# Kernel optimization log

Hardware: AMD Instinct MI355X
Metric: run time of the kernel (lower is better)

Reference implementation:

```python
import jax, jax.numpy as jnp
import numpy as np

N_NODES = 50000
D = 128
L = 3  # layers
R = 4  # relations
E = 200000  # edges per relation
LN_EPS = 1e-5
NEG_SLOPE = 0.2


def setup_inputs() -> dict:
    key = jax.random.key(0)
    ks = jax.random.split(key, 12)
    s = 1.0 / np.sqrt(D)  # xavier-ish scale
    return {
        "h": jax.random.normal(ks[0], (N_NODES, D), jnp.float32),
        "edge_src": jax.random.randint(ks[1], (R, E), 0, N_NODES, jnp.int32),
        "edge_dst": jax.random.randint(ks[2], (R, E), 0, N_NODES, jnp.int32),
        "W_src": jax.random.normal(ks[3], (L, R, D, D), jnp.float32) * s,
        "W_dst": jax.random.normal(ks[4], (L, R, D, D), jnp.float32) * s,
        "attn_l": jax.random.normal(ks[5], (L, R, D), jnp.float32) * s,
        "attn_r": jax.random.normal(ks[6], (L, R, D), jnp.float32) * s,
        "gat_bias": jax.random.normal(ks[7], (L, R, D), jnp.float32) * 0.02,
        "ntype_bias": jax.random.normal(ks[8], (L, D), jnp.float32) * 0.02,
        "ln_gamma": jnp.ones((L, D), jnp.float32),
        "ln_beta": jnp.zeros((L, D), jnp.float32),
    }


def _gat_rel(x, Wsrc, Wdst, al, ar, b, src, dst):
    # single-head DGL GATConv with bipartite (src, dst) feats (same node set here)
    n = x.shape[0]
    hs = x @ Wsrc  # [N, D] projected source feats
    hd = x @ Wdst  # [N, D] projected dest feats
    el = (hs * al).sum(-1)  # [N]
    er = (hd * ar).sum(-1)  # [N]
    e = jax.nn.leaky_relu(el[src] + er[dst], NEG_SLOPE)  # [E]
    # edge softmax over incoming edges of each dst node
    m = jax.lax.stop_gradient(jax.ops.segment_max(e, dst, num_segments=n))
    a = jnp.exp(e - m[dst])
    denom = jax.ops.segment_sum(a, dst, num_segments=n)
    w = a / denom[dst]  # [E] attention weights
    out = jax.ops.segment_sum(hs[src] * w[:, None], dst, num_segments=n)  # [N, D]
    return out + b


def _layer_norm(x, g, b):
    mu = x.mean(-1, keepdims=True)
    var = ((x - mu) ** 2).mean(-1, keepdims=True)
    return (x - mu) * jax.lax.rsqrt(var + LN_EPS) * g + b


def reference(h, edge_src, edge_dst, W_src, W_dst, attn_l, attn_r,
              gat_bias, ntype_bias, ln_gamma, ln_beta):
    x = h
    n_layers = W_src.shape[0]
    gat_vmapped = jax.vmap(_gat_rel, in_axes=(None, 0, 0, 0, 0, 0, 0, 0))
    for l in range(n_layers):
        rel_out = gat_vmapped(x, W_src[l], W_dst[l], attn_l[l], attn_r[l],
                              gat_bias[l], edge_src, edge_dst)  # [R, N, D]
        hsum = rel_out.sum(0) + ntype_bias[l]  # HeteroGraphConv 'sum' + ntype bias
        if l < n_layers - 1:
            hsum = jax.nn.relu(hsum)  # activation on all but final layer
        # mean over heads (num_heads=1) is identity; then per-layer LayerNorm
        x = _layer_norm(hsum, ln_gamma[l], ln_beta[l])
    return x
```

## Files before the change

kernel.cpp:

```cpp
#include <hip/hip_runtime.h>

#define NN 50000
#define DIM 128
#define NREL 4
#define NEDGE 200000
#define NLAYER 3
#define SNB 196

typedef short s16x8 __attribute__((ext_vector_type(8)));
typedef float f32x4 __attribute__((ext_vector_type(4)));

__device__ __forceinline__ unsigned short f2bf(float f) {
    union { float f; unsigned u; } c; c.f = f;
    unsigned u = c.u + 0x7fffu + ((c.u >> 16) & 1u);
    return (unsigned short)(u >> 16);
}
__device__ __forceinline__ float lo_bf(unsigned u) {
    union { float f; unsigned u; } c; c.u = u << 16; return c.f;
}
__device__ __forceinline__ float hi_bf(unsigned u) {
    union { float f; unsigned u; } c; c.u = u & 0xffff0000u; return c.f;
}

__global__ __launch_bounds__(256) void k_constf(float* __restrict__ out, int n, float v) {
    int i = blockIdx.x * 256 + threadIdx.x;
    if (i < n) out[i] = v;
}

__global__ __launch_bounds__(256) void k_count(const int* __restrict__ dst, int* __restrict__ counts) {
    int r = blockIdx.y;
    int i = blockIdx.x * 256 + threadIdx.x;
    if (i < NEDGE) {
        int d = dst[r * NEDGE + i];
        if ((unsigned)d < NN) atomicAdd(&counts[r * NN + d], 1);
    }
}

__global__ __launch_bounds__(256) void k_s1(const int* __restrict__ counts, int* __restrict__ bsum) {
    int r = blockIdx.y, b = blockIdx.x;
    int i = b * 256 + threadIdx.x;
    int v = (i < NN) ? counts[r * NN + i] : 0;
    #pragma unroll
    for (int m = 1; m < 64; m <<= 1) v += __shfl_xor(v, m);
    __shared__ int ws[4];
    int wid = threadIdx.x >> 6, lane = threadIdx.x & 63;
    if (lane == 0) ws[wid] = v;
    __syncthreads();
    if (threadIdx.x == 0) bsum[r * SNB + b] = ws[0] + ws[1] + ws[2] + ws[3];
}

__global__ __launch_bounds__(256) void k_s2(const int* __restrict__ bsum, int* __restrict__ boff) {
    int r = threadIdx.x >> 6;
    int lane = threadIdx.x & 63;
    int carry = 0;
    for (int c0 = 0; c0 < SNB; c0 += 64) {
        int b = c0 + lane;
        int v = (b < SNB) ? bsum[r * SNB + b] : 0;
        int inc = v;
        #pragma unroll
        for (int d = 1; d < 64; d <<= 1) {
            int t = __shfl_up(inc, d);
            if (lane >= d) inc += t;
        }
        if (b < SNB) boff[r * SNB + b] = carry + inc - v;
        carry += __shfl(inc, 63);
    }
}

__global__ __launch_bounds__(256) void k_s3(const int* __restrict__ counts, const int* __restrict__ boff,
                                            int* __restrict__ row_ptr) {
    int r = blockIdx.y, b = blockIdx.x;
    int i = b * 256 + threadIdx.x;
    int v = (i < NN) ? counts[r * NN + i] : 0;
    int lane = threadIdx.x & 63, wid = threadIdx.x >> 6;
    int inc = v;
    #pragma unroll
    for (int d = 1; d < 64; d <<= 1) {
        int t = __shfl_up(inc, d);
        if (lane >= d) inc += t;
    }
    __shared__ int ws[4];
    if (lane == 63) ws[wid] = inc;
    __syncthreads();
    int woff = 0;
    #pragma unroll
    for (int w = 0; w < 4; ++w) woff += (w < wid) ? ws[w] : 0;
    if (i < NN) row_ptr[r * (NN + 1) + i] = boff[r * SNB + b] + woff + inc - v;
    if (b == 0 && threadIdx.x == 0) row_ptr[r * (NN + 1) + NN] = NEDGE;
}

__global__ __launch_bounds__(256) void k_copynext(const int* __restrict__ row_ptr, int* __restrict__ nxt) {
    int r = blockIdx.y;
    int i = blockIdx.x * 256 + threadIdx.x;
    if (i < NN) nxt[r * NN + i] = row_ptr[r * (NN + 1) + i];
}

__global__ __launch_bounds__(256) void k_fill(const int* __restrict__ src, const int* __restrict__ dst,
                                              int* __restrict__ nxt, int* __restrict__ csr) {
    int r = blockIdx.y;
    int i = blockIdx.x * 256 + threadIdx.x;
    if (i < NEDGE) {
        int d = dst[r * NEDGE + i];
        if ((unsigned)d >= NN) return;
        int pos = atomicAdd(&nxt[r * NN + d], 1);
        if ((unsigned)pos < NEDGE) csr[r * NEDGE + pos] = src[r * NEDGE + i];
    }
}

__global__ __launch_bounds__(256) void k_prep(const float* __restrict__ Wsrc,
                                              const float* __restrict__ Wdst,
                                              const float* __restrict__ al,
                                              const float* __restrict__ ar,
                                              const float* __restrict__ ntb,
                                              const float* __restrict__ gb,
                                              const float* __restrict__ x,
                                              unsigned short* __restrict__ wf,
                                              float* __restrict__ wl,
                                              float* __restrict__ wr,
                                              float* __restrict__ biasc,
                                              unsigned short* __restrict__ xb) {
    int b = blockIdx.x;
    const int PL = NLAYER * 512;
    if (b < PL) {
        int l = b / 512;
        int t = b % 512;
        if (t < 256) {
            int idx = t * 256 + threadIdx.x;
            int jj = idx & 7, lane = (idx >> 3) & 63, s = (idx >> 9) & 3, tt = (idx >> 11) & 7, r = idx >> 14;
            int k = s * 32 + ((lane >> 4) << 3) + jj;
            int n = tt * 16 + (lane & 15);
            wf[l * 65536 + idx] = f2bf(Wsrc[((size_t)(l * NREL + r) * DIM + k) * DIM + n]);
        } else if (t < 384) {
            int gw = (t - 256) * 4 + (threadIdx.x >> 6);
            int lane = threadIdx.x & 63;
            int r = gw >> 7, k = gw & 127;
            const float* wrow = Wsrc + (((size_t)(l * NREL + r) * DIM + k) * DIM);
            const float* arow = al + (l * NREL + r) * DIM;
            float s = wrow[lane * 2] * arow[lane * 2] + wrow[lane * 2 + 1] * arow[lane * 2 + 1];
            #pragma unroll
            for (int m = 1; m < 64; m <<= 1) s += __shfl_xor(s, m);
            if (lane == 0) wl[l * 512 + gw] = s;
        } else {
            int gw = (t - 384) * 4 + (threadIdx.x >> 6);
            int lane = threadIdx.x & 63;
            int r = gw >> 7, k = gw & 127;
            const float* wrow = Wdst + (((size_t)(l * NREL + r) * DIM + k) * DIM);
            const float* arow = ar + (l * NREL + r) * DIM;
            float s = wrow[lane * 2] * arow[lane * 2] + wrow[lane * 2 + 1] * arow[lane * 2 + 1];
            #pragma unroll
            for (int m = 1; m < 64; m <<= 1) s += __shfl_xor(s, m);
            if (lane == 0) wr[l * 512 + gw] = s;
        }
    } else if (b < PL + 2) {
        int t = (b - PL) * 256 + threadIdx.x;
        if (t < NLAYER * DIM) {
            int l = t >> 7, k = t & 127;
            float s = ntb[t];
            #pragma unroll
            for (int r = 0; r < NREL; ++r) s += gb[(l * NREL + r) * DIM + k];
            biasc[t] = s;
        }
    } else {
        int i = ((b - PL - 2) * 256 + threadIdx.x) * 4;
        f32x4 v = *(const f32x4*)(x + i);
        unsigned short o[4];
        #pragma unroll
        for (int j = 0; j < 4; ++j) o[j] = f2bf(v[j]);
        *(ushort2*)(xb + i) = make_ushort2(o[0], o[1]);
        *(ushort2*)(xb + i + 2) = make_ushort2(o[2], o[3]);
    }
}

__global__ __launch_bounds__(256) void k_er0(const float* __restrict__ x,
                                             const float* __restrict__ wl,
                                             const float* __restrict__ wr,
                                             float* __restrict__ el,
                                             float* __restrict__ er) {
    int oct = threadIdx.x >> 3, ol = threadIdx.x & 7;
    int n = blockIdx.x * 32 + oct;
    if (n >= NN) return;
    int f0 = ol * 16;
    const float* xp = x + (size_t)n * DIM + f0;
    f32x4 xv[4];
    #pragma unroll
    for (int k = 0; k < 4; ++k) xv[k] = *(const f32x4*)(xp + 4 * k);
    #pragma unroll
    for (int r = 0; r < NREL; ++r) {
        float sl = 0.f, sr = 0.f;
        #pragma unroll
        for (int k = 0; k < 4; ++k) {
            f32x4 lv = *(const f32x4*)(wl + r * DIM + f0 + 4 * k);
            f32x4 rv = *(const f32x4*)(wr + r * DIM + f0 + 4 * k);
            sl += xv[k][0] * lv[0] + xv[k][1] * lv[1] + xv[k][2] * lv[2] + xv[k][3] * lv[3];
            sr += xv[k][0] * rv[0] + xv[k][1] * rv[1] + xv[k][2] * rv[2] + xv[k][3] * rv[3];
        }
        sl += __shfl_xor(sl, 1); sl += __shfl_xor(sl, 2); sl += __shfl_xor(sl, 4);
        sr += __shfl_xor(sr, 1); sr += __shfl_xor(sr, 2); sr += __shfl_xor(sr, 4);
        if (ol == 0) { el[r * NN + n] = sl; er[r * NN + n] = sr; }
    }
}

__global__ __launch_bounds__(256) void k_fused(const unsigned short* __restrict__ xb,
                                               const float* __restrict__ el,
                                               const float* __restrict__ er,
                                               const int* __restrict__ row_ptr,
                                               const int* __restrict__ csr,
                                               const unsigned short* __restrict__ wf,
                                               const float* __restrict__ biasc,
                                               const float* __restrict__ lng,
                                               const float* __restrict__ lnb,
                                               const float* __restrict__ wl,
                                               const float* __restrict__ wr,
                                               float* __restrict__ dout,
                                               unsigned short* __restrict__ xb2,
                                               float* __restrict__ el2,
                                               float* __restrict__ er2,
                                               int l, int last) {
    __shared__ s16x8 lds_a[16 * 64];
    int tid = threadIdx.x;

    {
        int pair = tid >> 2;
        int ol   = tid & 3;
        int nd   = pair >> 2;
        int r    = pair & 3;
        int n    = blockIdx.x * 16 + nd;
        int f0   = ol * 32;

        int start = row_ptr[r * (NN + 1) + n];
        int end   = row_ptr[r * (NN + 1) + n + 1];
        if (start < 0) start = 0;
        if (end > NEDGE) end = NEDGE;
        int deg = end - start;

        float ern = er[r * NN + n];
        const int* cp = csr + r * NEDGE;
        const float* elp = el + r * NN;

        f32x4 av[8] = {{0,0,0,0},{0,0,0,0},{0,0,0,0},{0,0,0,0},
                       {0,0,0,0},{0,0,0,0},{0,0,0,0},{0,0,0,0}};
        float denom = 0.f;
        if (deg > 0) {
            int s0 = cp[start]; if ((unsigned)s0 >= NN) s0 = 0;
            float e0 = elp[s0];
            const uint4* hp = (const uint4*)(xb + (size_t)s0 * DIM + f0);
            uint4 xa = hp[0], xbv = hp[1], xc = hp[2], xd = hp[3];
            for (int e = 0; e < deg; ++e) {
                int i1 = start + e + 1; i1 = (i1 < end) ? i1 : start;
                int s1 = cp[i1]; if ((unsigned)s1 >= NN) s1 = 0;
                float e1 = elp[s1];
                const uint4* hp1 = (const uint4*)(xb + (size_t)s1 * DIM + f0);
                uint4 ya = hp1[0], yb = hp1[1], yc = hp1[2], yd = hp1[3];

                float ev = e0 + ern;
                ev = ev >= 0.f ? ev : 0.2f * ev;
                ev = fminf(fmaxf(ev, -60.f), 60.f);
                float p = __expf(ev);
                denom += p;
                av[0][0] += p * lo_bf(xa.x); av[0][1] += p * hi_bf(xa.x);
                av[0][2] += p * lo_bf(xa.y); av[0][3] += p * hi_bf(xa.y);
                av[1][0] += p * lo_bf(xa.z); av[1][1] += p * hi_bf(xa.z);
                av[1][2] += p * lo_bf(xa.w); av[1][3] += p * hi_bf(xa.w);
                av[2][0] += p * lo_bf(xbv.x); av[2][1] += p * hi_bf(xbv.x);
                av[2][2] += p * lo_bf(xbv.y); av[2][3] += p * hi_bf(xbv.y);
                av[3][0] += p * lo_bf(xbv.z); av[3][1] += p * hi_bf(xbv.z);
                av[3][2] += p * lo_bf(xbv.w); av[3][3] += p * hi_bf(xbv.w);
                av[4][0] += p * lo_bf(xc.x); av[4][1] += p * hi_bf(xc.x);
                av[4][2] += p * lo_bf(xc.y); av[4][3] += p * hi_bf(xc.y);
                av[5][0] += p * lo_bf(xc.z); av[5][1] += p * hi_bf(xc.z);
                av[5][2] += p * lo_bf(xc.w); av[5][3] += p * hi_bf(xc.w);
                av[6][0] += p * lo_bf(xd.x); av[6][1] += p * hi_bf(xd.x);
                av[6][2] += p * lo_bf(xd.y); av[6][3] += p * hi_bf(xd.y);
                av[7][0] += p * lo_bf(xd.z); av[7][1] += p * hi_bf(xd.z);
                av[7][2] += p * lo_bf(xd.w); av[7][3] += p * hi_bf(xd.w);
                e0 = e1; xa = ya; xbv = yb; xc = yc; xd = yd;
            }
        }
        float inv = (deg > 0) ? (1.0f / denom) : 0.f;
        #pragma unroll
        for (int q = 0; q < 4; ++q) {
            s16x8 o;
            #pragma unroll
            for (int j = 0; j < 4; ++j) {
                o[j]     = (short)f2bf(av[2 * q][j] * inv);
                o[j + 4] = (short)f2bf(av[2 * q + 1][j] * inv);
            }
            lds_a[(r * 4 + ol) * 64 + q * 16 + nd] = o;
        }
    }
    __syncthreads();

    int wv = tid >> 6, lane = tid & 63;
    int quad = lane >> 4, n16 = lane & 15;
    f32x4 acc0 = {0.f, 0.f, 0.f, 0.f}, acc1 = {0.f, 0.f, 0.f, 0.f};
    {
        const s16x8* wfp = (const s16x8*)wf + (size_t)l * NREL * 2048;
        int t0c = wv * 2, t1c = wv * 2 + 1;
        #pragma unroll
        for (int sp = 0; sp < 16; ++sp) {
            s16x8 a = lds_a[sp * 64 + lane];
            const s16x8* wb = wfp + (size_t)(sp >> 2) * 2048;
            int sl = sp & 3;
            s16x8 b0 = wb[(t0c * 4 + sl) * 64 + lane];
            s16x8 b1 = wb[(t1c * 4 + sl) * 64 + lane];
            acc0 = __builtin_amdgcn_mfma_f32_16x16x32_bf16(a, b0, acc0, 0, 0, 0);
            acc1 = __builtin_amdgcn_mfma_f32_16x16x32_bf16(a, b1, acc1, 0, 0, 0);
        }
    }
    __syncthreads();
    float* Cl = (float*)lds_a;
    {
        int t0c = wv * 2, t1c = wv * 2 + 1;
        #pragma unroll
        for (int reg = 0; reg < 4; ++reg) {
            int row = quad * 4 + reg;
            Cl[row * DIM + t0c * 16 + n16] = acc0[reg];
            Cl[row * DIM + t1c * 16 + n16] = acc1[reg];
        }
    }
    __syncthreads();

    {
        int nd2 = tid >> 4;
        int sub = tid & 15;
        int f   = sub * 8;
        int n2  = blockIdx.x * 16 + nd2;

        float t[8];
        #pragma unroll
        for (int j = 0; j < 8; ++j) t[j] = Cl[nd2 * DIM + f + j] + biasc[l * DIM + f + j];
        if (!last) {
            #pragma unroll
            for (int j = 0; j < 8; ++j) t[j] = fmaxf(t[j], 0.f);
        }
        float s1 = 0.f;
        #pragma unroll
        for (int j = 0; j < 8; ++j) s1 += t[j];
        s1 += __shfl_xor(s1, 1); s1 += __shfl_xor(s1, 2);
        s1 += __shfl_xor(s1, 4); s1 += __shfl_xor(s1, 8);
        float mean = s1 * (1.0f / 128.0f);
        float s2 = 0.f;
        #pragma unroll
        for (int j = 0; j < 8; ++j) { t[j] -= mean; s2 += t[j] * t[j]; }
        s2 += __shfl_xor(s2, 1); s2 += __shfl_xor(s2, 2);
        s2 += __shfl_xor(s2, 4); s2 += __shfl_xor(s2, 8);
        float rs = rsqrtf(s2 * (1.0f / 128.0f) + 1e-5f);

        float y[8];
        #pragma unroll
        for (int j = 0; j < 8; ++j)
            y[j] = t[j] * rs * lng[l * DIM + f + j] + lnb[l * DIM + f + j];

        if (last) {
            float* op = dout + (size_t)n2 * DIM + f;
            f32x4 v0, v1;
            v0[0] = y[0]; v0[1] = y[1]; v0[2] = y[2]; v0[3] = y[3];
            v1[0] = y[4]; v1[1] = y[5]; v1[2] = y[6]; v1[3] = y[7];
            *(f32x4*)op = v0;
            *(f32x4*)(op + 4) = v1;
        } else {
            unsigned pk[4];
            #pragma unroll
            for (int j = 0; j < 4; ++j)
                pk[j] = (unsigned)f2bf(y[2 * j]) | ((unsigned)f2bf(y[2 * j + 1]) << 16);
            uint4 v; v.x = pk[0]; v.y = pk[1]; v.z = pk[2]; v.w = pk[3];
            *(uint4*)(xb2 + (size_t)n2 * DIM + f) = v;

            const float* wlp = wl + (l + 1) * 512;
            const float* wrp = wr + (l + 1) * 512;
            #pragma unroll
            for (int rp = 0; rp < NREL; ++rp) {
                float sl_ = 0.f, sr_ = 0.f;
                #pragma unroll
                for (int j = 0; j < 8; ++j) {
                    sl_ += y[j] * wlp[rp * DIM + f + j];
                    sr_ += y[j] * wrp[rp * DIM + f + j];
                }
                sl_ += __shfl_xor(sl_, 1); sl_ += __shfl_xor(sl_, 2);
                sl_ += __shfl_xor(sl_, 4); sl_ += __shfl_xor(sl_, 8);
                sr_ += __shfl_xor(sr_, 1); sr_ += __shfl_xor(sr_, 2);
                sr_ += __shfl_xor(sr_, 4); sr_ += __shfl_xor(sr_, 8);
                if (sub == 0) {
                    el2[rp * NN + n2] = sl_;
                    er2[rp * NN + n2] = sr_;
                }
            }
        }
    }
}

extern "C" void kernel_launch(void* const* d_in, const int* in_sizes, int n_in,
                              void* d_out, int out_size, void* d_ws, size_t ws_size,
                              hipStream_t stream) {
    const float* h        = (const float*)d_in[0];
    const int*   edge_src = (const int*)d_in[1];
    const int*   edge_dst = (const int*)d_in[2];
    const float* W_src    = (const float*)d_in[3];
    const float* W_dst    = (const float*)d_in[4];
    const float* attn_l   = (const float*)d_in[5];
    const float* attn_r   = (const float*)d_in[6];
    const float* gat_bias = (const float*)d_in[7];
    const float* ntype_b  = (const float*)d_in[8];
    const float* ln_g     = (const float*)d_in[9];
    const float* ln_b     = (const float*)d_in[10];

    if (n_in < 11) return;
    if (in_sizes[0] != NN * DIM) return;
    if (in_sizes[1] != NREL * NEDGE || in_sizes[2] != NREL * NEDGE) return;
    if (in_sizes[3] != NLAYER * NREL * DIM * DIM || in_sizes[4] != NLAYER * NREL * DIM * DIM) return;
    if (in_sizes[5] != NLAYER * NREL * DIM || in_sizes[6] != NLAYER * NREL * DIM) return;
    if (in_sizes[7] != NLAYER * NREL * DIM || in_sizes[8] != NLAYER * DIM) return;
    if (out_size != NN * DIM) return;

    auto align256 = [](size_t x) { return (x + 255) & ~(size_t)255; };
    size_t szElEr = align256((size_t)NREL * NN * 4);
    size_t szXbf  = align256((size_t)NN * DIM * 2);
    size_t szWlr  = align256((size_t)NLAYER * 512 * 4);
    size_t szBc   = align256((size_t)NLAYER * DIM * 4);
    size_t szWf   = align256((size_t)NLAYER * NREL * DIM * DIM * 2);
    size_t szRp   = align256((size_t)NREL * (NN + 1) * 4);
    size_t szNxt  = align256((size_t)NREL * NN * 4);
    size_t szCsr  = align256((size_t)NREL * NEDGE * 4);
    size_t szScn  = align256((size_t)NREL * SNB * 4) * 2;
    size_t need = 4 * szElEr + 2 * szXbf + 2 * szWlr + szBc + szWf + szRp + szNxt + szCsr + szScn;

    if (ws_size < need) {
        k_constf<<<(NN * DIM + 255) / 256, 256, 0, stream>>>((float*)d_out, NN * DIM, 100.0f);
        return;
    }

    char* base = (char*)d_ws;
    size_t off = 0;
    auto alloc = [&](size_t bytes) -> char* { char* p = base + off; off += align256(bytes); return p; };

    float* el   = (float*)alloc((size_t)NREL * NN * 4);
    float* er   = (float*)alloc((size_t)NREL * NN * 4);
    float* el2  = (float*)alloc((size_t)NREL * NN * 4);
    float* er2  = (float*)alloc((size_t)NREL * NN * 4);
    unsigned short* xbf  = (unsigned short*)alloc((size_t)NN * DIM * 2);
    unsigned short* xbf2 = (unsigned short*)alloc((size_t)NN * DIM * 2);
    float* wl    = (float*)alloc((size_t)NLAYER * 512 * 4);
    float* wr    = (float*)alloc((size_t)NLAYER * 512 * 4);
    float* biasc = (float*)alloc((size_t)NLAYER * DIM * 4);
    unsigned short* wfrag = (unsigned short*)alloc((size_t)NLAYER * NREL * DIM * DIM * 2);
    int* rowp = (int*)alloc((size_t)NREL * (NN + 1) * 4);
    int* nxt  = (int*)alloc((size_t)NREL * NN * 4);
    int* csr  = (int*)alloc((size_t)NREL * NEDGE * 4);
    int* bsum = (int*)alloc((size_t)NREL * SNB * 4);
    int* boff = (int*)alloc((size_t)NREL * SNB * 4);

    (void)hipMemsetAsync(nxt, 0, (size_t)NREL * NN * 4, stream);
    k_count<<<dim3((NEDGE + 255) / 256, NREL), 256, 0, stream>>>(edge_dst, nxt);
    k_s1<<<dim3(SNB, NREL), 256, 0, stream>>>(nxt, bsum);
    k_s2<<<1, 256, 0, stream>>>(bsum, boff);
    k_s3<<<dim3(SNB, NREL), 256, 0, stream>>>(nxt, boff, rowp);
    k_copynext<<<dim3((NN + 255) / 256, NREL), 256, 0, stream>>>(rowp, nxt);
    k_fill<<<dim3((NEDGE + 255) / 256, NREL), 256, 0, stream>>>(edge_src, edge_dst, nxt, csr);
    k_prep<<<NLAYER * 512 + 2 + NN * DIM / 1024, 256, 0, stream>>>(
        W_src, W_dst, attn_l, attn_r, ntype_b, gat_bias, h, wfrag, wl, wr, biasc, xbf);
    k_er0<<<(NN + 31) / 32, 256, 0, stream>>>(h, wl, wr, el, er);

    float* dout = (float*)d_out;
    k_fused<<<NN / 16, 256, 0, stream>>>(xbf, el, er, rowp, csr, wfrag, biasc, ln_g, ln_b,
                                         wl, wr, dout, xbf2, el2, er2, 0, 0);
    k_fused<<<NN / 16, 256, 0, stream>>>(xbf2, el2, er2, rowp, csr, wfrag, biasc, ln_g, ln_b,
                                         wl, wr, dout, xbf, el, er, 1, 0);
    k_fused<<<NN / 16, 256, 0, stream>>>(xbf, el, er, rowp, csr, wfrag, biasc, ln_g, ln_b,
                                         wl, wr, dout, xbf2, el2, er2, 2, 1);
}
```

Measured before the change: 348.9 us.

## Split edge gather across two lane groups and widen fused kernel to 512 threads

The fused GAT kernel now runs 512 threads per block. Each (node, relation, feature-slice) gets two lanes that take alternating incoming edges, and their partial sums are combined with a cross-lane shuffle. This roughly halves the serial gather chain per lane, giving more memory-level parallelism in the latency-bound aggregation. The MFMA and LayerNorm stages are redistributed across 8 waves to match. The CSR copy kernel is also folded into the scan kernel, saving a launch, at the cost of higher register pressure and extra shuffle reductions.

```diff
diff --git a/kernel.cpp b/kernel.cpp
--- a/kernel.cpp
+++ b/kernel.cpp
@@ -68,7 +68,7 @@
 }
 
 __global__ __launch_bounds__(256) void k_s3(const int* __restrict__ counts, const int* __restrict__ boff,
-                                            int* __restrict__ row_ptr) {
+                                            int* __restrict__ row_ptr, int* __restrict__ nxt) {
     int r = blockIdx.y, b = blockIdx.x;
     int i = b * 256 + threadIdx.x;
     int v = (i < NN) ? counts[r * NN + i] : 0;
@@ -85,14 +85,12 @@
     int woff = 0;
     #pragma unroll
     for (int w = 0; w < 4; ++w) woff += (w < wid) ? ws[w] : 0;
-    if (i < NN) row_ptr[r * (NN + 1) + i] = boff[r * SNB + b] + woff + inc - v;
+    if (i < NN) {
+        int ex = boff[r * SNB + b] + woff + inc - v;
+        row_ptr[r * (NN + 1) + i] = ex;
+        nxt[r * NN + i] = ex;
+    }
     if (b == 0 && threadIdx.x == 0) row_ptr[r * (NN + 1) + NN] = NEDGE;
-}
-
-__global__ __launch_bounds__(256) void k_copynext(const int* __restrict__ row_ptr, int* __restrict__ nxt) {
-    int r = blockIdx.y;
-    int i = blockIdx.x * 256 + threadIdx.x;
-    if (i < NN) nxt[r * NN + i] = row_ptr[r * (NN + 1) + i];
 }
 
 __global__ __launch_bounds__(256) void k_fill(const int* __restrict__ src, const int* __restrict__ dst,
@@ -200,7 +198,7 @@
     }
 }
 
-__global__ __launch_bounds__(256) void k_fused(const unsigned short* __restrict__ xb,
+__global__ __launch_bounds__(512) void k_fused(const unsigned short* __restrict__ xb,
                                                const float* __restrict__ el,
                                                const float* __restrict__ er,
                                                const int* __restrict__ row_ptr,
@@ -220,12 +218,14 @@
     int tid = threadIdx.x;
 
     {
-        int pair = tid >> 2;
-        int ol   = tid & 3;
+        int pair = tid >> 3;
+        int ol   = tid & 7;
+        int g    = ol >> 2;
+        int fl   = ol & 3;
         int nd   = pair >> 2;
         int r    = pair & 3;
         int n    = blockIdx.x * 16 + nd;
-        int f0   = ol * 32;
+        int f0   = fl * 32;
 
         int start = row_ptr[r * (NN + 1) + n];
         int end   = row_ptr[r * (NN + 1) + n + 1];
@@ -240,19 +240,20 @@
         f32x4 av[8] = {{0,0,0,0},{0,0,0,0},{0,0,0,0},{0,0,0,0},
                        {0,0,0,0},{0,0,0,0},{0,0,0,0},{0,0,0,0}};
         float denom = 0.f;
-        if (deg > 0) {
-            int s0 = cp[start]; if ((unsigned)s0 >= NN) s0 = 0;
-            float e0 = elp[s0];
+        int e = start + g;
+        if (e < end) {
+            int s0 = cp[e]; if ((unsigned)s0 >= NN) s0 = 0;
+            float e0v = elp[s0];
             const uint4* hp = (const uint4*)(xb + (size_t)s0 * DIM + f0);
             uint4 xa = hp[0], xbv = hp[1], xc = hp[2], xd = hp[3];
-            for (int e = 0; e < deg; ++e) {
-                int i1 = start + e + 1; i1 = (i1 < end) ? i1 : start;
+            for (; e < end; e += 2) {
+                int i1 = e + 2; i1 = (i1 < end) ? i1 : start;
                 int s1 = cp[i1]; if ((unsigned)s1 >= NN) s1 = 0;
-                float e1 = elp[s1];
+                float e1v = elp[s1];
                 const uint4* hp1 = (const uint4*)(xb + (size_t)s1 * DIM + f0);
                 uint4 ya = hp1[0], yb = hp1[1], yc = hp1[2], yd = hp1[3];
 
-                float ev = e0 + ern;
+                float ev = e0v + ern;
                 ev = ev >= 0.f ? ev : 0.2f * ev;
                 ev = fminf(fmaxf(ev, -60.f), 60.f);
                 float p = __expf(ev);
@@ -273,98 +274,99 @@
                 av[6][2] += p * lo_bf(xd.y); av[6][3] += p * hi_bf(xd.y);
                 av[7][0] += p * lo_bf(xd.z); av[7][1] += p * hi_bf(xd.z);
                 av[7][2] += p * lo_bf(xd.w); av[7][3] += p * hi_bf(xd.w);
-                e0 = e1; xa = ya; xbv = yb; xc = yc; xd = yd;
+                e0v = e1v; xa = ya; xbv = yb; xc = yc; xd = yd;
             }
         }
+        denom += __shfl_xor(denom, 4);
+        #pragma unroll
+        for (int q = 0; q < 8; ++q) {
+            #pragma unroll
+            for (int j = 0; j < 4; ++j) av[q][j] += __shfl_xor(av[q][j], 4);
+        }
         float inv = (deg > 0) ? (1.0f / denom) : 0.f;
-        #pragma unroll
-        for (int q = 0; q < 4; ++q) {
-            s16x8 o;
-            #pragma unroll
-            for (int j = 0; j < 4; ++j) {
-                o[j]     = (short)f2bf(av[2 * q][j] * inv);
-                o[j + 4] = (short)f2bf(av[2 * q + 1][j] * inv);
+        if (g == 0) {
+            #pragma unroll
+            for (int q = 0; q < 4; ++q) {
+                s16x8 o;
+                #pragma unroll
+                for (int j = 0; j < 4; ++j) {
+                    o[j]     = (short)f2bf(av[2 * q][j] * inv);
+                    o[j + 4] = (short)f2bf(av[2 * q + 1][j] * inv);
+                }
+                lds_a[(r * 4 + fl) * 64 + q * 16 + nd] = o;
             }
-            lds_a[(r * 4 + ol) * 64 + q * 16 + nd] = o;
         }
     }
     __syncthreads();
 
     int wv = tid >> 6, lane = tid & 63;
     int quad = lane >> 4, n16 = lane & 15;
-    f32x4 acc0 = {0.f, 0.f, 0.f, 0.f}, acc1 = {0.f, 0.f, 0.f, 0.f};
+    f32x4 acc = {0.f, 0.f, 0.f, 0.f};
     {
         const s16x8* wfp = (const s16x8*)wf + (size_t)l * NREL * 2048;
-        int t0c = wv * 2, t1c = wv * 2 + 1;
         #pragma unroll
         for (int sp = 0; sp < 16; ++sp) {
             s16x8 a = lds_a[sp * 64 + lane];
             const s16x8* wb = wfp + (size_t)(sp >> 2) * 2048;
             int sl = sp & 3;
-            s16x8 b0 = wb[(t0c * 4 + sl) * 64 + lane];
-            s16x8 b1 = wb[(t1c * 4 + sl) * 64 + lane];
-            acc0 = __builtin_amdgcn_mfma_f32_16x16x32_bf16(a, b0, acc0, 0, 0, 0);
-            acc1 = __builtin_amdgcn_mfma_f32_16x16x32_bf16(a, b1, acc1, 0, 0, 0);
+            s16x8 b = wb[(wv * 4 + sl) * 64 + lane];
+            acc = __builtin_amdgcn_mfma_f32_16x16x32_bf16(a, b, acc, 0, 0, 0);
         }
     }
     __syncthreads();
     float* Cl = (float*)lds_a;
     {
-        int t0c = wv * 2, t1c = wv * 2 + 1;
         #pragma unroll
         for (int reg = 0; reg < 4; ++reg) {
             int row = quad * 4 + reg;
-            Cl[row * DIM + t0c * 16 + n16] = acc0[reg];
-            Cl[row * DIM + t1c * 16 + n16] = acc1[reg];
+            Cl[row * DIM + wv * 16 + n16] = acc[reg];
         }
     }
     __syncthreads();
 
     {
-        int nd2 = tid >> 4;
-        int sub = tid & 15;
-        int f   = sub * 8;
+        int nd2 = tid >> 5;
+        int sub = tid & 31;
+        int f   = sub * 4;
         int n2  = blockIdx.x * 16 + nd2;
 
-        float t[8];
-        #pragma unroll
-        for (int j = 0; j < 8; ++j) t[j] = Cl[nd2 * DIM + f + j] + biasc[l * DIM + f + j];
+        float t[4];
+        #pragma unroll
+        for (int j = 0; j < 4; ++j) t[j] = Cl[nd2 * DIM + f + j] + biasc[l * DIM + f + j];
         if (!last) {
             #pragma unroll
-            for (int j = 0; j < 8; ++j) t[j] = fmaxf(t[j], 0.f);
+            for (int j = 0; j < 4; ++j) t[j] = fmaxf(t[j], 0.f);
         }
         float s1 = 0.f;
         #pragma unroll
-        for (int j = 0; j < 8; ++j) s1 += t[j];
+        for (int j = 0; j < 4; ++j) s1 += t[j];
         s1 += __shfl_xor(s1, 1); s1 += __shfl_xor(s1, 2);
         s1 += __shfl_xor(s1, 4); s1 += __shfl_xor(s1, 8);
+        s1 += __shfl_xor(s1, 16);
         float mean = s1 * (1.0f / 128.0f);
         float s2 = 0.f;
         #pragma unroll
-        for (int j = 0; j < 8; ++j) { t[j] -= mean; s2 += t[j] * t[j]; }
+        for (int j = 0; j < 4; ++j) { t[j] -= mean; s2 += t[j] * t[j]; }
         s2 += __shfl_xor(s2, 1); s2 += __shfl_xor(s2, 2);
         s2 += __shfl_xor(s2, 4); s2 += __shfl_xor(s2, 8);
+        s2 += __shfl_xor(s2, 16);
         float rs = rsqrtf(s2 * (1.0f / 128.0f) + 1e-5f);
 
-        float y[8];
-        #pragma unroll
-        for (int j = 0; j < 8; ++j)
+        float y[4];
+        #pragma unroll
+        for (int j = 0; j < 4; ++j)
             y[j] = t[j] * rs * lng[l * DIM + f + j] + lnb[l * DIM + f + j];
 
         if (last) {
             float* op = dout + (size_t)n2 * DIM + f;
-            f32x4 v0, v1;
+            f32x4 v0;
             v0[0] = y[0]; v0[1] = y[1]; v0[2] = y[2]; v0[3] = y[3];
-            v1[0] = y[4]; v1[1] = y[5]; v1[2] = y[6]; v1[3] = y[7];
             *(f32x4*)op = v0;
-            *(f32x4*)(op + 4) = v1;
         } else {
-            unsigned pk[4];
-            #pragma unroll
-            for (int j = 0; j < 4; ++j)
-                pk[j] = (unsigned)f2bf(y[2 * j]) | ((unsigned)f2bf(y[2 * j + 1]) << 16);
-            uint4 v; v.x = pk[0]; v.y = pk[1]; v.z = pk[2]; v.w = pk[3];
-            *(uint4*)(xb2 + (size_t)n2 * DIM + f) = v;
+            unsigned pk0 = (unsigned)f2bf(y[0]) | ((unsigned)f2bf(y[1]) << 16);
+            unsigned pk1 = (unsigned)f2bf(y[2]) | ((unsigned)f2bf(y[3]) << 16);
+            uint2 v; v.x = pk0; v.y = pk1;
+            *(uint2*)(xb2 + (size_t)n2 * DIM + f) = v;
 
             const float* wlp = wl + (l + 1) * 512;
             const float* wrp = wr + (l + 1) * 512;
@@ -372,14 +374,16 @@
             for (int rp = 0; rp < NREL; ++rp) {
                 float sl_ = 0.f, sr_ = 0.f;
                 #pragma unroll
-                for (int j = 0; j < 8; ++j) {
+                for (int j = 0; j < 4; ++j) {
                     sl_ += y[j] * wlp[rp * DIM + f + j];
                     sr_ += y[j] * wrp[rp * DIM + f + j];
                 }
                 sl_ += __shfl_xor(sl_, 1); sl_ += __shfl_xor(sl_, 2);
                 sl_ += __shfl_xor(sl_, 4); sl_ += __shfl_xor(sl_, 8);
+                sl_ += __shfl_xor(sl_, 16);
                 sr_ += __shfl_xor(sr_, 1); sr_ += __shfl_xor(sr_, 2);
                 sr_ += __shfl_xor(sr_, 4); sr_ += __shfl_xor(sr_, 8);
+                sr_ += __shfl_xor(sr_, 16);
                 if (sub == 0) {
                     el2[rp * NN + n2] = sl_;
                     er2[rp * NN + n2] = sr_;
@@ -453,18 +457,17 @@
     k_count<<<dim3((NEDGE + 255) / 256, NREL), 256, 0, stream>>>(edge_dst, nxt);
     k_s1<<<dim3(SNB, NREL), 256, 0, stream>>>(nxt, bsum);
     k_s2<<<1, 256, 0, stream>>>(bsum, boff);
-    k_s3<<<dim3(SNB, NREL), 256, 0, stream>>>(nxt, boff, rowp);
-    k_copynext<<<dim3((NN + 255) / 256, NREL), 256, 0, stream>>>(rowp, nxt);
+    k_s3<<<dim3(SNB, NREL), 256, 0, stream>>>(nxt, boff, rowp, nxt);
     k_fill<<<dim3((NEDGE + 255) / 256, NREL), 256, 0, stream>>>(edge_src, edge_dst, nxt, csr);
     k_prep<<<NLAYER * 512 + 2 + NN * DIM / 1024, 256, 0, stream>>>(
         W_src, W_dst, attn_l, attn_r, ntype_b, gat_bias, h, wfrag, wl, wr, biasc, xbf);
     k_er0<<<(NN + 31) / 32, 256, 0, stream>>>(h, wl, wr, el, er);
 
     float* dout = (float*)d_out;
-    k_fused<<<NN / 16, 256, 0, stream>>>(xbf, el, er, rowp, csr, wfrag, biasc, ln_g, ln_b,
+    k_fused<<<NN / 16, 512, 0, stream>>>(xbf, el, er, rowp, csr, wfrag, biasc, ln_g, ln_b,
                                          wl, wr, dout, xbf2, el2, er2, 0, 0);
-    k_fused<<<NN / 16, 256, 0, stream>>>(xbf2, el2, er2, rowp, csr, wfrag, biasc, ln_g, ln_b,
+    k_fused<<<NN / 16, 512, 0, stream>>>(xbf2, el2, er2, rowp, csr, wfrag, biasc, ln_g, ln_b,
                                          wl, wr, dout, xbf, el, er, 1, 0);
-    k_fused<<<NN / 16, 256, 0, stream>>>(xbf, el, er, rowp, csr, wfrag, biasc, ln_g, ln_b,
+    k_fused<<<NN / 16, 512, 0, stream>>>(xbf, el, er, rowp, csr, wfrag, biasc, ln_g, ln_b,
                                          wl, wr, dout, xbf2, el2, er2, 2, 1);
 }
```

Result: slower. 400.7 us (+14.9%).

## Fuse preprocessing kernels and sort nodes by max in-degree for load balance

Applied to the files above, without the earlier changes.

Merges the CSR-building and prep kernels into fewer launches: count fused into prep, block-sum fused with the layer-0 attention-logit kernel, and the block-offset scan folded into the final scan. It also adds a degree histogram, a scan and a scatter that build a permutation of nodes grouped by their maximum per-relation in-degree. The fused layer kernels process nodes in that order, so each 16-node block holds nodes of similar degree and warp divergence drops. This adds three small kernels and an indirection through perm, and loses node locality for the stores.

```diff
diff --git a/kernel.cpp b/kernel.cpp
--- a/kernel.cpp
+++ b/kernel.cpp
@@ -6,6 +6,12 @@
 #define NEDGE 200000
 #define NLAYER 3
 #define SNB 196
+#define EBLK ((NEDGE + 255) / 256)
+#define PREPB (NLAYER * 512 + 2 + NN * DIM / 1024)
+#define S1B (SNB * NREL)
+#define ER0B ((NN + 31) / 32)
+#define FILLB (EBLK * NREL)
+#define HISTB ((NN + 255) / 256)
 
 typedef short s16x8 __attribute__((ext_vector_type(8)));
 typedef float f32x4 __attribute__((ext_vector_type(4)));
@@ -27,98 +33,20 @@
     if (i < n) out[i] = v;
 }
 
-__global__ __launch_bounds__(256) void k_count(const int* __restrict__ dst, int* __restrict__ counts) {
-    int r = blockIdx.y;
-    int i = blockIdx.x * 256 + threadIdx.x;
-    if (i < NEDGE) {
-        int d = dst[r * NEDGE + i];
-        if ((unsigned)d < NN) atomicAdd(&counts[r * NN + d], 1);
-    }
-}
-
-__global__ __launch_bounds__(256) void k_s1(const int* __restrict__ counts, int* __restrict__ bsum) {
-    int r = blockIdx.y, b = blockIdx.x;
-    int i = b * 256 + threadIdx.x;
-    int v = (i < NN) ? counts[r * NN + i] : 0;
-    #pragma unroll
-    for (int m = 1; m < 64; m <<= 1) v += __shfl_xor(v, m);
-    __shared__ int ws[4];
-    int wid = threadIdx.x >> 6, lane = threadIdx.x & 63;
-    if (lane == 0) ws[wid] = v;
-    __syncthreads();
-    if (threadIdx.x == 0) bsum[r * SNB + b] = ws[0] + ws[1] + ws[2] + ws[3];
-}
-
-__global__ __launch_bounds__(256) void k_s2(const int* __restrict__ bsum, int* __restrict__ boff) {
-    int r = threadIdx.x >> 6;
-    int lane = threadIdx.x & 63;
-    int carry = 0;
-    for (int c0 = 0; c0 < SNB; c0 += 64) {
-        int b = c0 + lane;
-        int v = (b < SNB) ? bsum[r * SNB + b] : 0;
-        int inc = v;
-        #pragma unroll
-        for (int d = 1; d < 64; d <<= 1) {
-            int t = __shfl_up(inc, d);
-            if (lane >= d) inc += t;
-        }
-        if (b < SNB) boff[r * SNB + b] = carry + inc - v;
-        carry += __shfl(inc, 63);
-    }
-}
-
-__global__ __launch_bounds__(256) void k_s3(const int* __restrict__ counts, const int* __restrict__ boff,
-                                            int* __restrict__ row_ptr) {
-    int r = blockIdx.y, b = blockIdx.x;
-    int i = b * 256 + threadIdx.x;
-    int v = (i < NN) ? counts[r * NN + i] : 0;
-    int lane = threadIdx.x & 63, wid = threadIdx.x >> 6;
-    int inc = v;
-    #pragma unroll
-    for (int d = 1; d < 64; d <<= 1) {
-        int t = __shfl_up(inc, d);
-        if (lane >= d) inc += t;
-    }
-    __shared__ int ws[4];
-    if (lane == 63) ws[wid] = inc;
-    __syncthreads();
-    int woff = 0;
-    #pragma unroll
-    for (int w = 0; w < 4; ++w) woff += (w < wid) ? ws[w] : 0;
-    if (i < NN) row_ptr[r * (NN + 1) + i] = boff[r * SNB + b] + woff + inc - v;
-    if (b == 0 && threadIdx.x == 0) row_ptr[r * (NN + 1) + NN] = NEDGE;
-}
-
-__global__ __launch_bounds__(256) void k_copynext(const int* __restrict__ row_ptr, int* __restrict__ nxt) {
-    int r = blockIdx.y;
-    int i = blockIdx.x * 256 + threadIdx.x;
-    if (i < NN) nxt[r * NN + i] = row_ptr[r * (NN + 1) + i];
-}
-
-__global__ __launch_bounds__(256) void k_fill(const int* __restrict__ src, const int* __restrict__ dst,
-                                              int* __restrict__ nxt, int* __restrict__ csr) {
-    int r = blockIdx.y;
-    int i = blockIdx.x * 256 + threadIdx.x;
-    if (i < NEDGE) {
-        int d = dst[r * NEDGE + i];
-        if ((unsigned)d >= NN) return;
-        int pos = atomicAdd(&nxt[r * NN + d], 1);
-        if ((unsigned)pos < NEDGE) csr[r * NEDGE + pos] = src[r * NEDGE + i];
-    }
-}
-
-__global__ __launch_bounds__(256) void k_prep(const float* __restrict__ Wsrc,
-                                              const float* __restrict__ Wdst,
-                                              const float* __restrict__ al,
-                                              const float* __restrict__ ar,
-                                              const float* __restrict__ ntb,
-                                              const float* __restrict__ gb,
-                                              const float* __restrict__ x,
-                                              unsigned short* __restrict__ wf,
-                                              float* __restrict__ wl,
-                                              float* __restrict__ wr,
-                                              float* __restrict__ biasc,
-                                              unsigned short* __restrict__ xb) {
+__global__ __launch_bounds__(256) void k_prep_count(const float* __restrict__ Wsrc,
+                                                    const float* __restrict__ Wdst,
+                                                    const float* __restrict__ al,
+                                                    const float* __restrict__ ar,
+                                                    const float* __restrict__ ntb,
+                                                    const float* __restrict__ gb,
+                                                    const float* __restrict__ x,
+                                                    const int* __restrict__ dst,
+                                                    unsigned short* __restrict__ wf,
+                                                    float* __restrict__ wl,
+                                                    float* __restrict__ wr,
+                                                    float* __restrict__ biasc,
+                                                    unsigned short* __restrict__ xb,
+                                                    int* __restrict__ counts) {
     int b = blockIdx.x;
     const int PL = NLAYER * 512;
     if (b < PL) {
@@ -160,7 +88,7 @@
             for (int r = 0; r < NREL; ++r) s += gb[(l * NREL + r) * DIM + k];
             biasc[t] = s;
         }
-    } else {
+    } else if (b < PREPB) {
         int i = ((b - PL - 2) * 256 + threadIdx.x) * 4;
         f32x4 v = *(const f32x4*)(x + i);
         unsigned short o[4];
@@ -168,35 +96,153 @@
         for (int j = 0; j < 4; ++j) o[j] = f2bf(v[j]);
         *(ushort2*)(xb + i) = make_ushort2(o[0], o[1]);
         *(ushort2*)(xb + i + 2) = make_ushort2(o[2], o[3]);
-    }
-}
-
-__global__ __launch_bounds__(256) void k_er0(const float* __restrict__ x,
-                                             const float* __restrict__ wl,
-                                             const float* __restrict__ wr,
-                                             float* __restrict__ el,
-                                             float* __restrict__ er) {
-    int oct = threadIdx.x >> 3, ol = threadIdx.x & 7;
-    int n = blockIdx.x * 32 + oct;
-    if (n >= NN) return;
-    int f0 = ol * 16;
-    const float* xp = x + (size_t)n * DIM + f0;
-    f32x4 xv[4];
+    } else {
+        int idx = b - PREPB;
+        int r = idx / EBLK;
+        int i = (idx % EBLK) * 256 + threadIdx.x;
+        if (i < NEDGE) {
+            int d = dst[r * NEDGE + i];
+            if ((unsigned)d < NN) atomicAdd(&counts[r * NN + d], 1);
+        }
+    }
+}
+
+__global__ __launch_bounds__(256) void k_s1_er0(const int* __restrict__ counts,
+                                                int* __restrict__ bsum,
+                                                const float* __restrict__ x,
+                                                const float* __restrict__ wl,
+                                                const float* __restrict__ wr,
+                                                float* __restrict__ el,
+                                                float* __restrict__ er) {
+    __shared__ int ws[4];
+    int blk = blockIdx.x;
+    if (blk < S1B) {
+        int r = blk / SNB, b = blk % SNB;
+        int i = b * 256 + threadIdx.x;
+        int v = (i < NN) ? counts[r * NN + i] : 0;
+        #pragma unroll
+        for (int m = 1; m < 64; m <<= 1) v += __shfl_xor(v, m);
+        int wid = threadIdx.x >> 6, lane = threadIdx.x & 63;
+        if (lane == 0) ws[wid] = v;
+        __syncthreads();
+        if (threadIdx.x == 0) bsum[r * SNB + b] = ws[0] + ws[1] + ws[2] + ws[3];
+    } else {
+        int oct = threadIdx.x >> 3, ol = threadIdx.x & 7;
+        int n = (blk - S1B) * 32 + oct;
+        if (n >= NN) return;
+        int f0 = ol * 16;
+        const float* xp = x + (size_t)n * DIM + f0;
+        f32x4 xv[4];
+        #pragma unroll
+        for (int k = 0; k < 4; ++k) xv[k] = *(const f32x4*)(xp + 4 * k);
+        #pragma unroll
+        for (int r = 0; r < NREL; ++r) {
+            float sl = 0.f, sr = 0.f;
+            #pragma unroll
+            for (int k = 0; k < 4; ++k) {
+                f32x4 lv = *(const f32x4*)(wl + r * DIM + f0 + 4 * k);
+                f32x4 rv = *(const f32x4*)(wr + r * DIM + f0 + 4 * k);
+                sl += xv[k][0] * lv[0] + xv[k][1] * lv[1] + xv[k][2] * lv[2] + xv[k][3] * lv[3];
+                sr += xv[k][0] * rv[0] + xv[k][1] * rv[1] + xv[k][2] * rv[2] + xv[k][3] * rv[3];
+            }
+            sl += __shfl_xor(sl, 1); sl += __shfl_xor(sl, 2); sl += __shfl_xor(sl, 4);
+            sr += __shfl_xor(sr, 1); sr += __shfl_xor(sr, 2); sr += __shfl_xor(sr, 4);
+            if (ol == 0) { el[r * NN + n] = sl; er[r * NN + n] = sr; }
+        }
+    }
+}
+
+__global__ __launch_bounds__(256) void k_s3b(const int* __restrict__ counts,
+                                             const int* __restrict__ bsum,
+                                             int* __restrict__ row_ptr,
+                                             int* __restrict__ nxt) {
+    int r = blockIdx.y, b = blockIdx.x;
+    int i = b * 256 + threadIdx.x;
+    int v = (i < NN) ? counts[r * NN + i] : 0;
+    int lane = threadIdx.x & 63, wid = threadIdx.x >> 6;
+    int inc = v;
     #pragma unroll
-    for (int k = 0; k < 4; ++k) xv[k] = *(const f32x4*)(xp + 4 * k);
+    for (int d = 1; d < 64; d <<= 1) {
+        int t = __shfl_up(inc, d);
+        if (lane >= d) inc += t;
+    }
+    int part = 0;
+    for (int j = threadIdx.x; j < b; j += 256) part += bsum[r * SNB + j];
     #pragma unroll
-    for (int r = 0; r < NREL; ++r) {
-        float sl = 0.f, sr = 0.f;
-        #pragma unroll
-        for (int k = 0; k < 4; ++k) {
-            f32x4 lv = *(const f32x4*)(wl + r * DIM + f0 + 4 * k);
-            f32x4 rv = *(const f32x4*)(wr + r * DIM + f0 + 4 * k);
-            sl += xv[k][0] * lv[0] + xv[k][1] * lv[1] + xv[k][2] * lv[2] + xv[k][3] * lv[3];
-            sr += xv[k][0] * rv[0] + xv[k][1] * rv[1] + xv[k][2] * rv[2] + xv[k][3] * rv[3];
-        }
-        sl += __shfl_xor(sl, 1); sl += __shfl_xor(sl, 2); sl += __shfl_xor(sl, 4);
-        sr += __shfl_xor(sr, 1); sr += __shfl_xor(sr, 2); sr += __shfl_xor(sr, 4);
-        if (ol == 0) { el[r * NN + n] = sl; er[r * NN + n] = sr; }
+    for (int m = 1; m < 64; m <<= 1) part += __shfl_xor(part, m);
+    __shared__ int ws[4], wsum[4];
+    if (lane == 63) ws[wid] = inc;
+    if (lane == 0) wsum[wid] = part;
+    __syncthreads();
+    int pref = wsum[0] + wsum[1] + wsum[2] + wsum[3];
+    int woff = 0;
+    #pragma unroll
+    for (int w = 0; w < 4; ++w) woff += (w < wid) ? ws[w] : 0;
+    if (i < NN) {
+        int ex = pref + woff + inc - v;
+        row_ptr[r * (NN + 1) + i] = ex;
+        nxt[r * NN + i] = ex;
+    }
+    if (b == 0 && threadIdx.x == 0) row_ptr[r * (NN + 1) + NN] = NEDGE;
+}
+
+__global__ __launch_bounds__(256) void k_fill_hist(const int* __restrict__ src,
+                                                   const int* __restrict__ dst,
+                                                   int* __restrict__ nxt,
+                                                   int* __restrict__ csr,
+                                                   const int* __restrict__ row_ptr,
+                                                   int* __restrict__ hist) {
+    int blk = blockIdx.x;
+    if (blk < FILLB) {
+        int r = blk / EBLK;
+        int i = (blk % EBLK) * 256 + threadIdx.x;
+        if (i < NEDGE) {
+            int d = dst[r * NEDGE + i];
+            if ((unsigned)d >= NN) return;
+            int pos = atomicAdd(&nxt[r * NN + d], 1);
+            if ((unsigned)pos < NEDGE) csr[r * NEDGE + pos] = src[r * NEDGE + i];
+        }
+    } else {
+        int n = (blk - FILLB) * 256 + threadIdx.x;
+        if (n < NN) {
+            int dmax = 0;
+            #pragma unroll
+            for (int r = 0; r < NREL; ++r) {
+                int dg = row_ptr[r * (NN + 1) + n + 1] - row_ptr[r * (NN + 1) + n];
+                dmax = max(dmax, dg);
+            }
+            if (dmax > 63) dmax = 63;
+            atomicAdd(&hist[dmax], 1);
+        }
+    }
+}
+
+__global__ __launch_bounds__(64) void k_hscan(const int* __restrict__ hist, int* __restrict__ cursors) {
+    int lane = threadIdx.x;
+    int v = hist[lane];
+    int inc = v;
+    #pragma unroll
+    for (int d = 1; d < 64; d <<= 1) {
+        int t = __shfl_up(inc, d);
+        if (lane >= d) inc += t;
+    }
+    cursors[lane] = inc - v;
+}
+
+__global__ __launch_bounds__(256) void k_scatter(const int* __restrict__ row_ptr,
+                                                 int* __restrict__ cursors,
+                                                 int* __restrict__ perm) {
+    int n = blockIdx.x * 256 + threadIdx.x;
+    if (n < NN) {
+        int dmax = 0;
+        #pragma unroll
+        for (int r = 0; r < NREL; ++r) {
+            int dg = row_ptr[r * (NN + 1) + n + 1] - row_ptr[r * (NN + 1) + n];
+            dmax = max(dmax, dg);
+        }
+        if (dmax > 63) dmax = 63;
+        int pos = atomicAdd(&cursors[dmax], 1);
+        if ((unsigned)pos < NN) perm[pos] = n;
     }
 }
 
@@ -211,6 +257,7 @@
                                                const float* __restrict__ lnb,
                                                const float* __restrict__ wl,
                                                const float* __restrict__ wr,
+                                               const int* __restrict__ perm,
                                                float* __restrict__ dout,
                                                unsigned short* __restrict__ xb2,
                                                float* __restrict__ el2,
@@ -224,7 +271,7 @@
         int ol   = tid & 3;
         int nd   = pair >> 2;
         int r    = pair & 3;
-        int n    = blockIdx.x * 16 + nd;
+        int n    = perm[blockIdx.x * 16 + nd];
         int f0   = ol * 32;
 
         int start = row_ptr[r * (NN + 1) + n];
@@ -324,7 +371,7 @@
         int nd2 = tid >> 4;
         int sub = tid & 15;
         int f   = sub * 8;
-        int n2  = blockIdx.x * 16 + nd2;
+        int n2  = perm[blockIdx.x * 16 + nd2];
 
         float t[8];
         #pragma unroll
@@ -421,8 +468,11 @@
     size_t szRp   = align256((size_t)NREL * (NN + 1) * 4);
     size_t szNxt  = align256((size_t)NREL * NN * 4);
     size_t szCsr  = align256((size_t)NREL * NEDGE * 4);
-    size_t szScn  = align256((size_t)NREL * SNB * 4) * 2;
-    size_t need = 4 * szElEr + 2 * szXbf + 2 * szWlr + szBc + szWf + szRp + szNxt + szCsr + szScn;
+    size_t szScn  = align256((size_t)NREL * SNB * 4);
+    size_t szHist = 256;
+    size_t szPerm = align256((size_t)NN * 4);
+    size_t need = 4 * szElEr + 2 * szXbf + 2 * szWlr + szBc + szWf + szRp + szNxt
+                + 2 * szHist + szPerm + szCsr + szScn;
 
     if (ws_size < need) {
         k_constf<<<(NN * DIM + 255) / 256, 256, 0, stream>>>((float*)d_out, NN * DIM, 100.0f);
@@ -445,26 +495,27 @@
     unsigned short* wfrag = (unsigned short*)alloc((size_t)NLAYER * NREL * DIM * DIM * 2);
     int* rowp = (int*)alloc((size_t)NREL * (NN + 1) * 4);
     int* nxt  = (int*)alloc((size_t)NREL * NN * 4);
+    int* hist = (int*)alloc(256);
+    int* cursors = (int*)alloc(256);
+    int* perm = (int*)alloc((size_t)NN * 4);
     int* csr  = (int*)alloc((size_t)NREL * NEDGE * 4);
     int* bsum = (int*)alloc((size_t)NREL * SNB * 4);
-    int* boff = (int*)alloc((size_t)NREL * SNB * 4);
-
-    (void)hipMemsetAsync(nxt, 0, (size_t)NREL * NN * 4, stream);
-    k_count<<<dim3((NEDGE + 255) / 256, NREL), 256, 0, stream>>>(edge_dst, nxt);
-    k_s1<<<dim3(SNB, NREL), 256, 0, stream>>>(nxt, bsum);
-    k_s2<<<1, 256, 0, stream>>>(bsum, boff);
-    k_s3<<<dim3(SNB, NREL), 256, 0, stream>>>(nxt, boff, rowp);
-    k_copynext<<<dim3((NN + 255) / 256, NREL), 256, 0, stream>>>(rowp, nxt);
-    k_fill<<<dim3((NEDGE + 255) / 256, NREL), 256, 0, stream>>>(edge_src, edge_dst, nxt, csr);
-    k_prep<<<NLAYER * 512 + 2 + NN * DIM / 1024, 256, 0, stream>>>(
-        W_src, W_dst, attn_l, attn_r, ntype_b, gat_bias, h, wfrag, wl, wr, biasc, xbf);
-    k_er0<<<(NN + 31) / 32, 256, 0, stream>>>(h, wl, wr, el, er);
+
+    (void)hipMemsetAsync(nxt, 0, (size_t)NREL * NN * 4 + 256, stream);
+    k_prep_count<<<PREPB + FILLB, 256, 0, stream>>>(
+        W_src, W_dst, attn_l, attn_r, ntype_b, gat_bias, h, edge_dst,
+        wfrag, wl, wr, biasc, xbf, nxt);
+    k_s1_er0<<<S1B + ER0B, 256, 0, stream>>>(nxt, bsum, h, wl, wr, el, er);
+    k_s3b<<<dim3(SNB, NREL), 256, 0, stream>>>(nxt, bsum, rowp, nxt);
+    k_fill_hist<<<FILLB + HISTB, 256, 0, stream>>>(edge_src, edge_dst, nxt, csr, rowp, hist);
+    k_hscan<<<1, 64, 0, stream>>>(hist, cursors);
+    k_scatter<<<HISTB, 256, 0, stream>>>(rowp, cursors, perm);
 
     float* dout = (float*)d_out;
     k_fused<<<NN / 16, 256, 0, stream>>>(xbf, el, er, rowp, csr, wfrag, biasc, ln_g, ln_b,
-                                         wl, wr, dout, xbf2, el2, er2, 0, 0);
+                                         wl, wr, perm, dout, xbf2, el2, er2, 0, 0);
     k_fused<<<NN / 16, 256, 0, stream>>>(xbf2, el2, er2, rowp, csr, wfrag, biasc, ln_g, ln_b,
-                                         wl, wr, dout, xbf, el, er, 1, 0);
+                                         wl, wr, perm, dout, xbf, el, er, 1, 0);
     k_fused<<<NN / 16, 256, 0, stream>>>(xbf, el, er, rowp, csr, wfrag, biasc, ln_g, ln_b,
-                                         wl, wr, dout, xbf2, el2, er2, 2, 1);
-}
+                                         wl, wr, perm, dout, xbf2, el2, er2, 2, 1);
+}
```

Result: slower. 806.3 us (+131.1%).
